# Kernel tuning notes

Hardware: AMD Instinct MI355X
Metric: run time of the kernel (lower is better)

## Reference

```python
import jax, jax.numpy as jnp
import numpy as np

N, E, F_IN, H, OUT, G = 40000, 640000, 128, 128, 10, 256


def setup_inputs() -> dict:
    key = jax.random.key(0)
    ks = jax.random.split(key, 8)
    x = jax.random.normal(ks[0], (N, F_IN), dtype=jnp.float32)
    edge_index = jax.random.randint(ks[1], (2, E), 0, N, dtype=jnp.int32)
    batch = jnp.sort(jax.random.randint(ks[2], (N,), 0, G, dtype=jnp.int32))
    W1 = jax.random.normal(ks[3], (F_IN, H), dtype=jnp.float32) / np.sqrt(F_IN)
    b1 = jnp.zeros((H,), dtype=jnp.float32)
    W2 = jax.random.normal(ks[4], (H, H), dtype=jnp.float32) / np.sqrt(H)
    b2 = jnp.zeros((H,), dtype=jnp.float32)
    Wfc = jax.random.normal(ks[5], (H, OUT), dtype=jnp.float32) / np.sqrt(H)
    bfc = jnp.zeros((OUT,), dtype=jnp.float32)
    return {"x": x, "edge_index": edge_index, "batch": batch,
            "W1": W1, "b1": b1, "W2": W2, "b2": b2, "Wfc": Wfc, "bfc": bfc}


def _gcn_conv(x, W, b, row, col, num_nodes):
    # x' = D^{-1/2} (A+I) D^{-1/2} (x W) + b   (self-loops already in row/col)
    xw = x @ W                                            # [N, H]
    ones = jnp.ones(row.shape[0], dtype=x.dtype)
    deg = jax.ops.segment_sum(ones, col, num_segments=num_nodes)
    dinv = jnp.where(deg > 0, jax.lax.rsqrt(jnp.maximum(deg, 1.0)), 0.0)
    norm = dinv[row] * dinv[col]                          # [E+N]
    msg = xw[row] * norm[:, None]                         # gather + scale
    return jax.ops.segment_sum(msg, col, num_segments=num_nodes) + b


def reference(x, edge_index, batch, W1, b1, W2, b2, Wfc, bfc):
    num_nodes = x.shape[0]
    loop = jnp.arange(num_nodes, dtype=edge_index.dtype)
    row = jnp.concatenate([edge_index[0], loop])
    col = jnp.concatenate([edge_index[1], loop])

    h = jax.nn.relu(_gcn_conv(x, W1, b1, row, col, num_nodes))
    h = jax.nn.relu(_gcn_conv(h, W2, b2, row, col, num_nodes))

    # global_mean_pool over graph ids
    sums = jax.ops.segment_sum(h, batch, num_segments=G)  # [G, H]
    cnt = jax.ops.segment_sum(jnp.ones(num_nodes, h.dtype), batch, num_segments=G)
    pooled = sums / jnp.maximum(cnt, 1.0)[:, None]

    logits = pooled @ Wfc + bfc                           # [G, OUT]
    return jax.nn.log_softmax(logits, axis=-1)
```

## Files before the change

### kernel.cpp

```cpp
#include <hip/hip_runtime.h>
#include <math.h>

#define H_DIM 128
#define OUT_DIM 10

typedef __attribute__((ext_vector_type(8))) __bf16 bf16x8;
typedef __attribute__((ext_vector_type(8))) unsigned short ushort8;
typedef __attribute__((ext_vector_type(4))) float f32x4;

__device__ inline unsigned short f2bf_rne(float f) {
    unsigned int u = __float_as_uint(f);
    unsigned int r = u + 0x7FFFu + ((u >> 16) & 1u);
    return (unsigned short)(r >> 16);
}
__device__ inline float bf_lo(unsigned int u) { return __uint_as_float(u << 16); }
__device__ inline float bf_hi(unsigned int u) { return __uint_as_float(u & 0xFFFF0000u); }

#define ACC4(gv, nv) do { \
    const unsigned int* _u = (const unsigned int*)&(gv); \
    ax[0] += bf_lo(_u[0]) * (nv); ay[0] += bf_hi(_u[0]) * (nv); \
    ax[1] += bf_lo(_u[1]) * (nv); ay[1] += bf_hi(_u[1]) * (nv); \
    ax[2] += bf_lo(_u[2]) * (nv); ay[2] += bf_hi(_u[2]) * (nv); \
    ax[3] += bf_lo(_u[3]) * (nv); ay[3] += bf_hi(_u[3]) * (nv); \
} while (0)

__device__ inline void gather_node(const int4* __restrict__ XW16,
                                   const int2* __restrict__ csr,
                                   int start, int end, int c, float dc2,
                                   int sub, int fl, int lane,
                                   float ax[4], float ay[4]) {
    {
        float s = (sub == 0) ? dc2 : 0.0f;
        int4 gs = XW16[(size_t)c * 16 + fl];
        const unsigned int* u = (const unsigned int*)&gs;
        ax[0] = bf_lo(u[0]) * s; ay[0] = bf_hi(u[0]) * s;
        ax[1] = bf_lo(u[1]) * s; ay[1] = bf_hi(u[1]) * s;
        ax[2] = bf_lo(u[2]) * s; ay[2] = bf_hi(u[2]) * s;
        ax[3] = bf_lo(u[3]) * s; ay[3] = bf_hi(u[3]) * s;
    }
    for (int base = start; base < end; base += 64) {
        int m = end - base; if (m > 64) m = 64;
        int2 ce; ce.x = c; ce.y = 0;
        if (lane < m) ce = csr[base + lane];
        int groups = (m + 3) >> 2;
        int g = 0;
        for (; g + 3 < groups; g += 4) {
            int j = g * 4 + sub;
            int r0 = __shfl(ce.x, j);      float n0 = __int_as_float(__shfl(ce.y, j));
            int r1 = __shfl(ce.x, j + 4);  float n1 = __int_as_float(__shfl(ce.y, j + 4));
            int r2 = __shfl(ce.x, j + 8);  float n2 = __int_as_float(__shfl(ce.y, j + 8));
            int r3 = __shfl(ce.x, j + 12); float n3 = __int_as_float(__shfl(ce.y, j + 12));
            int4 g0 = XW16[(size_t)r0 * 16 + fl];
            int4 g1 = XW16[(size_t)r1 * 16 + fl];
            int4 g2 = XW16[(size_t)r2 * 16 + fl];
            int4 g3 = XW16[(size_t)r3 * 16 + fl];
            ACC4(g0, n0); ACC4(g1, n1); ACC4(g2, n2); ACC4(g3, n3);
        }
        for (; g < groups; ++g) {
            int j = g * 4 + sub;
            int r = __shfl(ce.x, j); float n = __int_as_float(__shfl(ce.y, j));
            int4 gg = XW16[(size_t)r * 16 + fl];
            ACC4(gg, n);
        }
    }
    #pragma unroll
    for (int q = 0; q < 4; ++q) {
        ax[q] += __shfl_xor(ax[q], 16); ax[q] += __shfl_xor(ax[q], 32);
        ay[q] += __shfl_xor(ay[q], 16); ay[q] += __shfl_xor(ay[q], 32);
    }
}

__global__ __launch_bounds__(256) void prep_kernel(const float* __restrict__ W1,
                                                   const float* __restrict__ W2,
                                                   unsigned short* __restrict__ Wt1Hi,
                                                   unsigned short* __restrict__ Wt1Lo,
                                                   unsigned short* __restrict__ Wt2Hi,
                                                   unsigned short* __restrict__ Wt2Lo,
                                                   int hb,
                                                   const int* __restrict__ col,
                                                   int* __restrict__ cnt,
                                                   int* __restrict__ rank, int E) {
    if (blockIdx.x < (unsigned)hb) {
        int e = blockIdx.x * 256 + threadIdx.x;
        if (e < E) rank[e] = atomicAdd(&cnt[col[e]], 1);
    } else {
        int i = (blockIdx.x - hb) * 256 + threadIdx.x;
        const float* src   = (i < 16384) ? W1    : W2;
        unsigned short* dh = (i < 16384) ? Wt1Hi : Wt2Hi;
        unsigned short* dl = (i < 16384) ? Wt1Lo : Wt2Lo;
        int idx = i & 16383;
        int k = idx >> 7, n = idx & 127;
        float v = src[idx];
        unsigned short hbv = f2bf_rne(v);
        float hf = __uint_as_float((unsigned int)hbv << 16);
        unsigned short lb = f2bf_rne(v - hf);
        dh[n * H_DIM + k] = hbv;
        dl[n * H_DIM + k] = lb;
    }
}

__global__ __launch_bounds__(256) void scan_phase1(const int* __restrict__ cnt,
                                                   int* __restrict__ blockSums,
                                                   float* __restrict__ dinv, int N) {
    __shared__ int red[256];
    int base = blockIdx.x * 1024;
    int t = threadIdx.x;
    int s = 0;
    for (int i = 0; i < 4; ++i) {
        int idx = base + t * 4 + i;
        if (idx < N) {
            int cv = cnt[idx];
            s += cv;
            dinv[idx] = rsqrtf((float)cv + 1.0f);
        }
    }
    red[t] = s;
    __syncthreads();
    for (int d = 128; d > 0; d >>= 1) {
        if (t < d) red[t] += red[t + d];
        __syncthreads();
    }
    if (t == 0) blockSums[blockIdx.x] = red[0];
}

__global__ __launch_bounds__(256) void scan_phase23(const int* __restrict__ cnt,
                                                    const int* __restrict__ blockSums,
                                                    int* __restrict__ offs, int N, int B) {
    __shared__ int red[256];
    __shared__ int bsum[256];
    int base = blockIdx.x * 1024;
    int t = threadIdx.x;

    bsum[t] = (t < B && t < (int)blockIdx.x) ? blockSums[t] : 0;

    int v[4];
    int s = 0;
    for (int i = 0; i < 4; ++i) {
        int idx = base + t * 4 + i;
        v[i] = (idx < N) ? cnt[idx] : 0;
        s += v[i];
    }
    red[t] = s;
    __syncthreads();
    for (int d = 128; d > 0; d >>= 1) {
        if (t < d) bsum[t] += bsum[t + d];
        __syncthreads();
    }
    for (int d = 1; d < 256; d <<= 1) {
        int x = (t >= d) ? red[t - d] : 0;
        __syncthreads();
        red[t] += x;
        __syncthreads();
    }
    int run = bsum[0] + ((t == 0) ? 0 : red[t - 1]);
    for (int i = 0; i < 4; ++i) {
        int idx = base + t * 4 + i;
        if (idx < N) { offs[idx] = run; run += v[i]; }
    }
    if ((int)blockIdx.x == B - 1 && t == 255) offs[N] = run;
}

__global__ __launch_bounds__(256) void scatter_gemm1(
        const int* __restrict__ row, const int* __restrict__ col,
        const int* __restrict__ rank, const float* __restrict__ dinv,
        const int* __restrict__ offs, int2* __restrict__ csr, int E, int sb,
        const float* __restrict__ Xf,
        const unsigned short* __restrict__ WtHi, const unsigned short* __restrict__ WtLo,
        unsigned short* __restrict__ Yb, int N) {
    if (blockIdx.x < (unsigned)sb) {
        int e = blockIdx.x * 256 + threadIdx.x;
        if (e >= E) return;
        int r = row[e], c = col[e], rk = rank[e];
        int pos = offs[c] + rk;
        int2 p; p.x = r; p.y = __float_as_int(dinv[r] * dinv[c]);
        csr[pos] = p;
        return;
    }
    int blk  = blockIdx.x - sb;
    int lane = threadIdx.x & 63;
    int wv   = threadIdx.x >> 6;
    int m16  = lane & 15;
    int quad = lane >> 4;
    int nodeBase = blk * 32;

    f32x4 acc[2][2] = {};

    #pragma unroll
    for (int kt = 0; kt < 4; ++kt) {
        int k0 = kt * 32 + quad * 8;

        ushort8 aHi[2], aLo[2];
        #pragma unroll
        for (int mi = 0; mi < 2; ++mi) {
            int node = nodeBase + mi * 16 + m16;
            if (node >= N) node = N - 1;
            const float* p = Xf + (size_t)node * H_DIM + k0;
            f32x4 u = *(const f32x4*)p;
            f32x4 w = *(const f32x4*)(p + 4);
            float vv[8] = {u.x, u.y, u.z, u.w, w.x, w.y, w.z, w.w};
            #pragma unroll
            for (int j = 0; j < 8; ++j) {
                unsigned short hbv = f2bf_rne(vv[j]);
                aHi[mi][j] = hbv;
                aLo[mi][j] = f2bf_rne(vv[j] - __uint_as_float((unsigned int)hbv << 16));
            }
        }

        ushort8 bHi[2], bLo[2];
        #pragma unroll
        for (int ni = 0; ni < 2; ++ni) {
            int n = (wv * 2 + ni) * 16 + m16;
            size_t off = (size_t)n * H_DIM + k0;
            bHi[ni] = *(const ushort8*)(WtHi + off);
            bLo[ni] = *(const ushort8*)(WtLo + off);
        }

        #pragma unroll
        for (int mi = 0; mi < 2; ++mi)
            #pragma unroll
            for (int ni = 0; ni < 2; ++ni) {
                acc[mi][ni] = __builtin_amdgcn_mfma_f32_16x16x32_bf16(
                    __builtin_bit_cast(bf16x8, aHi[mi]),
                    __builtin_bit_cast(bf16x8, bHi[ni]), acc[mi][ni], 0, 0, 0);
                acc[mi][ni] = __builtin_amdgcn_mfma_f32_16x16x32_bf16(
                    __builtin_bit_cast(bf16x8, aLo[mi]),
                    __builtin_bit_cast(bf16x8, bHi[ni]), acc[mi][ni], 0, 0, 0);
                acc[mi][ni] = __builtin_amdgcn_mfma_f32_16x16x32_bf16(
                    __builtin_bit_cast(bf16x8, aHi[mi]),
                    __builtin_bit_cast(bf16x8, bLo[ni]), acc[mi][ni], 0, 0, 0);
            }
    }

    #pragma unroll
    for (int mi = 0; mi < 2; ++mi)
        #pragma unroll
        for (int r = 0; r < 4; ++r) {
            int node = nodeBase + mi * 16 + quad * 4 + r;
            if (node < N) {
                #pragma unroll
                for (int ni = 0; ni < 2; ++ni) {
                    int c = (wv * 2 + ni) * 16 + m16;
                    Yb[(size_t)node * H_DIM + c] = f2bf_rne(acc[mi][ni][r]);
                }
            }
        }
}

__global__ __launch_bounds__(256) void agg1_gemm2(
        const unsigned short* __restrict__ XWb,
        const float* __restrict__ dinv,
        const int2* __restrict__ csr,
        const int* __restrict__ offs,
        const float* __restrict__ bias,
        const unsigned short* __restrict__ WtHi,
        const unsigned short* __restrict__ WtLo,
        unsigned short* __restrict__ Yb,
        int N) {
    __shared__ __align__(16) unsigned short hrow[16][136];
    int lane = threadIdx.x & 63;
    int wv   = threadIdx.x >> 6;
    int sub  = lane >> 4;
    int fl   = lane & 15;
    int nodeBase = blockIdx.x * 16;
    const int4* XW16 = (const int4*)XWb;
    float4 b0 = ((const float4*)bias)[fl * 2];
    float4 b1 = ((const float4*)bias)[fl * 2 + 1];

    for (int i = 0; i < 4; ++i) {
        int c = nodeBase + wv * 4 + i;
        float ax[4] = {}, ay[4] = {};
        if (c < N) {
            int start = offs[c], end = offs[c + 1];
            float dc = dinv[c];
            gather_node(XW16, csr, start, end, c, dc * dc, sub, fl, lane, ax, ay);
            ax[0] = fmaxf(ax[0] + b0.x, 0.f); ay[0] = fmaxf(ay[0] + b0.y, 0.f);
            ax[1] = fmaxf(ax[1] + b0.z, 0.f); ay[1] = fmaxf(ay[1] + b0.w, 0.f);
            ax[2] = fmaxf(ax[2] + b1.x, 0.f); ay[2] = fmaxf(ay[2] + b1.y, 0.f);
            ax[3] = fmaxf(ax[3] + b1.z, 0.f); ay[3] = fmaxf(ay[3] + b1.w, 0.f);
        }
        if (sub == 0) {
            unsigned int o[4];
            #pragma unroll
            for (int q = 0; q < 4; ++q)
                o[q] = (unsigned int)f2bf_rne(ax[q]) | ((unsigned int)f2bf_rne(ay[q]) << 16);
            *(int4*)&hrow[wv * 4 + i][fl * 8] = *(const int4*)o;
        }
    }
    __syncthreads();

    int m16  = lane & 15;
    int quad = lane >> 4;
    f32x4 acc[2] = {};
    #pragma unroll
    for (int kt = 0; kt < 4; ++kt) {
        int k0 = kt * 32 + quad * 8;
        ushort8 a = *(const ushort8*)&hrow[m16][k0];
        #pragma unroll
        for (int ni = 0; ni < 2; ++ni) {
            int n = (wv * 2 + ni) * 16 + m16;
            size_t off = (size_t)n * H_DIM + k0;
            ushort8 bHi = *(const ushort8*)(WtHi + off);
            ushort8 bLo = *(const ushort8*)(WtLo + off);
            acc[ni] = __builtin_amdgcn_mfma_f32_16x16x32_bf16(
                __builtin_bit_cast(bf16x8, a),
                __builtin_bit_cast(bf16x8, bHi), acc[ni], 0, 0, 0);
            acc[ni] = __builtin_amdgcn_mfma_f32_16x16x32_bf16(
                __builtin_bit_cast(bf16x8, a),
                __builtin_bit_cast(bf16x8, bLo), acc[ni], 0, 0, 0);
        }
    }
    #pragma unroll
    for (int r = 0; r < 4; ++r) {
        int node = nodeBase + quad * 4 + r;
        if (node < N) {
            #pragma unroll
            for (int ni = 0; ni < 2; ++ni) {
                int cc = (wv * 2 + ni) * 16 + m16;
                Yb[(size_t)node * H_DIM + cc] = f2bf_rne(acc[ni][r]);
            }
        }
    }
}

__global__ __launch_bounds__(256) void agg_pool(const unsigned short* __restrict__ XWb,
                                                const float* __restrict__ dinv,
                                                const int2* __restrict__ csr,
                                                const int* __restrict__ offs,
                                                const float* __restrict__ bias,
                                                const int* __restrict__ batch,
                                                float* __restrict__ pooledSum, int N) {
    int wave = (blockIdx.x * 256 + threadIdx.x) >> 6;
    int lane = threadIdx.x & 63;
    int wv   = threadIdx.x >> 6;
    int sub  = lane >> 4;
    int fl   = lane & 15;
    bool active = wave < N;

    float ax[4] = {}, ay[4] = {};
    int c = wave;
    if (active) {
        int start = offs[c], end = offs[c + 1];
        float dc = dinv[c];
        gather_node((const int4*)XWb, csr, start, end, c, dc * dc, sub, fl, lane, ax, ay);
        float4 b0 = ((const float4*)bias)[fl * 2];
        float4 b1 = ((const float4*)bias)[fl * 2 + 1];
        ax[0] = fmaxf(ax[0] + b0.x, 0.f); ay[0] = fmaxf(ay[0] + b0.y, 0.f);
        ax[1] = fmaxf(ax[1] + b0.z, 0.f); ay[1] = fmaxf(ay[1] + b0.w, 0.f);
        ax[2] = fmaxf(ax[2] + b1.x, 0.f); ay[2] = fmaxf(ay[2] + b1.y, 0.f);
        ax[3] = fmaxf(ax[3] + b1.z, 0.f); ay[3] = fmaxf(ay[3] + b1.w, 0.f);
    }

    __shared__ float lacc[4][H_DIM];
    __shared__ int lg[4];
    if (lane == 0) lg[wv] = active ? batch[c] : -1;
    if (sub == 0) {
        float4 f0; f0.x = ax[0]; f0.y = ay[0]; f0.z = ax[1]; f0.w = ay[1];
        float4 f1; f1.x = ax[2]; f1.y = ay[2]; f1.z = ax[3]; f1.w = ay[3];
        ((float4*)&lacc[wv][fl * 8])[0] = f0;
        ((float4*)&lacc[wv][fl * 8])[1] = f1;
    }
    __syncthreads();
    int t = threadIdx.x;
    if (t < H_DIM) {
        float s = 0.f; int cur = -1;
        #pragma unroll
        for (int w = 0; w < 4; ++w) {
            int g = lg[w];
            if (g < 0) continue;
            if (g != cur) {
                if (cur >= 0) atomicAdd(&pooledSum[cur * H_DIM + t], s);
                s = 0.f; cur = g;
            }
            s += lacc[w][t];
        }
        if (cur >= 0) atomicAdd(&pooledSum[cur * H_DIM + t], s);
    }
}

__global__ __launch_bounds__(64) void head_kernel(const float* __restrict__ pooledSum,
                                                  const int* __restrict__ batch,
                                                  const float* __restrict__ Wfc,
                                                  const float* __restrict__ bfc,
                                                  float* __restrict__ out, int N) {
    __shared__ float sl[OUT_DIM + 2];
    __shared__ int bounds[2];
    int g = blockIdx.x;
    int j = threadIdx.x;
    if (j < 2) {
        int v = g + j;
        int lo = 0, hi = N;
        while (lo < hi) {
            int mid = (lo + hi) >> 1;
            if (batch[mid] < v) lo = mid + 1; else hi = mid;
        }
        bounds[j] = lo;
    }
    __syncthreads();
    int cnt = bounds[1] - bounds[0];
    float inv = 1.0f / (float)(cnt > 0 ? cnt : 1);
    if (j < OUT_DIM) {
        float acc = 0.f;
        const float* p = pooledSum + g * H_DIM;
        for (int k = 0; k < H_DIM; ++k) acc += p[k] * Wfc[k * OUT_DIM + j];
        sl[j] = acc * inv + bfc[j];
    }
    __syncthreads();
    if (j == 0) {
        float m = sl[0];
        for (int i = 1; i < OUT_DIM; ++i) m = fmaxf(m, sl[i]);
        float s = 0.f;
        for (int i = 0; i < OUT_DIM; ++i) s += expf(sl[i] - m);
        sl[OUT_DIM] = m + logf(s);
    }
    __syncthreads();
    if (j < OUT_DIM) out[g * OUT_DIM + j] = sl[j] - sl[OUT_DIM];
}

extern "C" void kernel_launch(void* const* d_in, const int* in_sizes, int n_in,
                              void* d_out, int out_size, void* d_ws, size_t ws_size,
                              hipStream_t stream) {
    const float* x     = (const float*)d_in[0];
    const int*   ei    = (const int*)  d_in[1];
    const int*   batch = (const int*)  d_in[2];
    const float* W1    = (const float*)d_in[3];
    const float* b1    = (const float*)d_in[4];
    const float* W2    = (const float*)d_in[5];
    const float* b2    = (const float*)d_in[6];
    const float* Wfc   = (const float*)d_in[7];
    const float* bfc   = (const float*)d_in[8];
    float* out = (float*)d_out;

    int N = in_sizes[2];
    int E = in_sizes[1] / 2;
    int G = out_size / OUT_DIM;
    const int* row = ei;
    const int* col = ei + E;

    char* wsb = (char*)d_ws;
    size_t nAlign = (size_t)((N + 256) / 256) * 256;
    size_t eAlign = (size_t)((E + 255) / 256) * 256;
    int*   cnt       = (int*)wsb;
    float* pooledSum = (float*)(cnt + nAlign);
    int*   offs      = (int*)(pooledSum + (size_t)G * H_DIM);
    int*   rank      = offs + nAlign;
    float* dinv      = (float*)(rank + eAlign);
    int2*  csr       = (int2*)(dinv + nAlign);
    unsigned short* Xb = (unsigned short*)(csr + E);
    unsigned short* Hb = Xb + (size_t)N * H_DIM;
    int* blockSums = (int*)(Hb + (size_t)N * H_DIM);
    unsigned short* Wt1Hi = (unsigned short*)(blockSums + 256);
    unsigned short* Wt1Lo = Wt1Hi + H_DIM * H_DIM;
    unsigned short* Wt2Hi = Wt1Lo + H_DIM * H_DIM;
    unsigned short* Wt2Lo = Wt2Hi + H_DIM * H_DIM;

    int scanBlocks = (N + 1023) / 1024;
    int histBlocks = (E + 255) / 256;
    int gemmBlocks = (N + 31) / 32;

    hipMemsetAsync(cnt, 0, (nAlign + (size_t)G * H_DIM) * sizeof(int), stream);

    prep_kernel<<<histBlocks + 128, 256, 0, stream>>>(
        W1, W2, Wt1Hi, Wt1Lo, Wt2Hi, Wt2Lo, histBlocks, col, cnt, rank, E);

    scan_phase1<<<scanBlocks, 256, 0, stream>>>(cnt, blockSums, dinv, N);
    scan_phase23<<<scanBlocks, 256, 0, stream>>>(cnt, blockSums, offs, N, scanBlocks);

    scatter_gemm1<<<histBlocks + gemmBlocks, 256, 0, stream>>>(
        row, col, rank, dinv, offs, csr, E, histBlocks,
        x, Wt1Hi, Wt1Lo, Xb, N);

    int ag1Blocks = (N + 15) / 16;
    agg1_gemm2<<<ag1Blocks, 256, 0, stream>>>(Xb, dinv, csr, offs, b1,
                                              Wt2Hi, Wt2Lo, Hb, N);

    int aggBlocks = (N + 3) / 4;
    agg_pool<<<aggBlocks, 256, 0, stream>>>(Hb, dinv, csr, offs, b2,
                                            batch, pooledSum, N);

    head_kernel<<<G, 64, 0, stream>>>(pooledSum, batch, Wfc, bfc, out, N);
}
```

Baseline: 222.3 us.

## Pack CSR entries into 32-bit index+fp16 norm and restructure agg1_gemm2 per-wave nodes

CSR entries are packed into one 32-bit word: the source index sits in the upper 16 bits and the edge norm is stored as fp16 in the lower 16 bits. This halves the CSR traffic in the scatter and in both aggregation kernels. agg1_gemm2 now uses 512-thread blocks with one node per wave, and the MFMA tile is zero-padded to 16 rows. The packing only holds for fewer than 65536 nodes and lowers norm precision to fp16, and the padded MFMA wastes half of its rows.

```diff
diff --git a/kernel.cpp b/kernel.cpp
--- a/kernel.cpp
+++ b/kernel.cpp
@@ -1,4 +1,5 @@
 #include <hip/hip_runtime.h>
+#include <hip/hip_fp16.h>
 #include <math.h>
 
 #define H_DIM 128
@@ -15,6 +16,9 @@
 }
 __device__ inline float bf_lo(unsigned int u) { return __uint_as_float(u << 16); }
 __device__ inline float bf_hi(unsigned int u) { return __uint_as_float(u & 0xFFFF0000u); }
+__device__ inline float h2f(unsigned int e) {
+    return __half2float(__ushort_as_half((unsigned short)(e & 0xFFFFu)));
+}
 
 #define ACC4(gv, nv) do { \
     const unsigned int* _u = (const unsigned int*)&(gv); \
@@ -25,7 +29,7 @@
 } while (0)
 
 __device__ inline void gather_node(const int4* __restrict__ XW16,
-                                   const int2* __restrict__ csr,
+                                   const unsigned int* __restrict__ csr,
                                    int start, int end, int c, float dc2,
                                    int sub, int fl, int lane,
                                    float ax[4], float ay[4]) {
@@ -40,26 +44,28 @@
     }
     for (int base = start; base < end; base += 64) {
         int m = end - base; if (m > 64) m = 64;
-        int2 ce; ce.x = c; ce.y = 0;
+        unsigned int ce = ((unsigned int)c) << 16;
         if (lane < m) ce = csr[base + lane];
         int groups = (m + 3) >> 2;
         int g = 0;
         for (; g + 3 < groups; g += 4) {
             int j = g * 4 + sub;
-            int r0 = __shfl(ce.x, j);      float n0 = __int_as_float(__shfl(ce.y, j));
-            int r1 = __shfl(ce.x, j + 4);  float n1 = __int_as_float(__shfl(ce.y, j + 4));
-            int r2 = __shfl(ce.x, j + 8);  float n2 = __int_as_float(__shfl(ce.y, j + 8));
-            int r3 = __shfl(ce.x, j + 12); float n3 = __int_as_float(__shfl(ce.y, j + 12));
-            int4 g0 = XW16[(size_t)r0 * 16 + fl];
-            int4 g1 = XW16[(size_t)r1 * 16 + fl];
-            int4 g2 = XW16[(size_t)r2 * 16 + fl];
-            int4 g3 = XW16[(size_t)r3 * 16 + fl];
+            unsigned int e0 = __shfl((int)ce, j);
+            unsigned int e1 = __shfl((int)ce, j + 4);
+            unsigned int e2 = __shfl((int)ce, j + 8);
+            unsigned int e3 = __shfl((int)ce, j + 12);
+            int4 g0 = XW16[(size_t)(e0 >> 16) * 16 + fl];
+            int4 g1 = XW16[(size_t)(e1 >> 16) * 16 + fl];
+            int4 g2 = XW16[(size_t)(e2 >> 16) * 16 + fl];
+            int4 g3 = XW16[(size_t)(e3 >> 16) * 16 + fl];
+            float n0 = h2f(e0), n1 = h2f(e1), n2 = h2f(e2), n3 = h2f(e3);
             ACC4(g0, n0); ACC4(g1, n1); ACC4(g2, n2); ACC4(g3, n3);
         }
         for (; g < groups; ++g) {
             int j = g * 4 + sub;
-            int r = __shfl(ce.x, j); float n = __int_as_float(__shfl(ce.y, j));
-            int4 gg = XW16[(size_t)r * 16 + fl];
+            unsigned int e = __shfl((int)ce, j);
+            int4 gg = XW16[(size_t)(e >> 16) * 16 + fl];
+            float n = h2f(e);
             ACC4(gg, n);
         }
     }
@@ -163,7 +169,7 @@
 __global__ __launch_bounds__(256) void scatter_gemm1(
         const int* __restrict__ row, const int* __restrict__ col,
         const int* __restrict__ rank, const float* __restrict__ dinv,
-        const int* __restrict__ offs, int2* __restrict__ csr, int E, int sb,
+        const int* __restrict__ offs, unsigned int* __restrict__ csr, int E, int sb,
         const float* __restrict__ Xf,
         const unsigned short* __restrict__ WtHi, const unsigned short* __restrict__ WtLo,
         unsigned short* __restrict__ Yb, int N) {
@@ -172,8 +178,9 @@
         if (e >= E) return;
         int r = row[e], c = col[e], rk = rank[e];
         int pos = offs[c] + rk;
-        int2 p; p.x = r; p.y = __float_as_int(dinv[r] * dinv[c]);
-        csr[pos] = p;
+        float norm = dinv[r] * dinv[c];
+        unsigned short nb = __half_as_ushort(__float2half(norm));
+        csr[pos] = (((unsigned int)r) << 16) | nb;
         return;
     }
     int blk  = blockIdx.x - sb;
@@ -246,10 +253,10 @@
         }
 }
 
-__global__ __launch_bounds__(256) void agg1_gemm2(
+__global__ __launch_bounds__(512, 8) void agg1_gemm2(
         const unsigned short* __restrict__ XWb,
         const float* __restrict__ dinv,
-        const int2* __restrict__ csr,
+        const unsigned int* __restrict__ csr,
         const int* __restrict__ offs,
         const float* __restrict__ bias,
         const unsigned short* __restrict__ WtHi,
@@ -261,70 +268,63 @@
     int wv   = threadIdx.x >> 6;
     int sub  = lane >> 4;
     int fl   = lane & 15;
-    int nodeBase = blockIdx.x * 16;
+    int nodeBase = blockIdx.x * 8;
+    int c = nodeBase + wv;
     const int4* XW16 = (const int4*)XWb;
-    float4 b0 = ((const float4*)bias)[fl * 2];
-    float4 b1 = ((const float4*)bias)[fl * 2 + 1];
-
-    for (int i = 0; i < 4; ++i) {
-        int c = nodeBase + wv * 4 + i;
-        float ax[4] = {}, ay[4] = {};
-        if (c < N) {
-            int start = offs[c], end = offs[c + 1];
-            float dc = dinv[c];
-            gather_node(XW16, csr, start, end, c, dc * dc, sub, fl, lane, ax, ay);
-            ax[0] = fmaxf(ax[0] + b0.x, 0.f); ay[0] = fmaxf(ay[0] + b0.y, 0.f);
-            ax[1] = fmaxf(ax[1] + b0.z, 0.f); ay[1] = fmaxf(ay[1] + b0.w, 0.f);
-            ax[2] = fmaxf(ax[2] + b1.x, 0.f); ay[2] = fmaxf(ay[2] + b1.y, 0.f);
-            ax[3] = fmaxf(ax[3] + b1.z, 0.f); ay[3] = fmaxf(ay[3] + b1.w, 0.f);
-        }
-        if (sub == 0) {
-            unsigned int o[4];
-            #pragma unroll
-            for (int q = 0; q < 4; ++q)
-                o[q] = (unsigned int)f2bf_rne(ax[q]) | ((unsigned int)f2bf_rne(ay[q]) << 16);
-            *(int4*)&hrow[wv * 4 + i][fl * 8] = *(const int4*)o;
-        }
+
+    float ax[4] = {}, ay[4] = {};
+    if (c < N) {
+        int start = offs[c], end = offs[c + 1];
+        float dc = dinv[c];
+        gather_node(XW16, csr, start, end, c, dc * dc, sub, fl, lane, ax, ay);
+        float4 b0 = ((const float4*)bias)[fl * 2];
+        float4 b1 = ((const float4*)bias)[fl * 2 + 1];
+        ax[0] = fmaxf(ax[0] + b0.x, 0.f); ay[0] = fmaxf(ay[0] + b0.y, 0.f);
+        ax[1] = fmaxf(ax[1] + b0.z, 0.f); ay[1] = fmaxf(ay[1] + b0.w, 0.f);
+        ax[2] = fmaxf(ax[2] + b1.x, 0.f); ay[2] = fmaxf(ay[2] + b1.y, 0.f);
+        ax[3] = fmaxf(ax[3] + b1.z, 0.f); ay[3] = fmaxf(ay[3] + b1.w, 0.f);
+    }
+    if (sub == 0) {
+        unsigned int o[4];
+        #pragma unroll
+        for (int q = 0; q < 4; ++q)
+            o[q] = (unsigned int)f2bf_rne(ax[q]) | ((unsigned int)f2bf_rne(ay[q]) << 16);
+        *(int4*)&hrow[wv][fl * 8] = *(const int4*)o;
+        int4 z; z.x = 0; z.y = 0; z.z = 0; z.w = 0;
+        *(int4*)&hrow[wv + 8][fl * 8] = z;
     }
     __syncthreads();
 
     int m16  = lane & 15;
     int quad = lane >> 4;
-    f32x4 acc[2] = {};
+    f32x4 acc = {};
     #pragma unroll
     for (int kt = 0; kt < 4; ++kt) {
         int k0 = kt * 32 + quad * 8;
         ushort8 a = *(const ushort8*)&hrow[m16][k0];
-        #pragma unroll
-        for (int ni = 0; ni < 2; ++ni) {
-            int n = (wv * 2 + ni) * 16 + m16;
-            size_t off = (size_t)n * H_DIM + k0;
-            ushort8 bHi = *(const ushort8*)(WtHi + off);
-            ushort8 bLo = *(const ushort8*)(WtLo + off);
-            acc[ni] = __builtin_amdgcn_mfma_f32_16x16x32_bf16(
-                __builtin_bit_cast(bf16x8, a),
-                __builtin_bit_cast(bf16x8, bHi), acc[ni], 0, 0, 0);
-            acc[ni] = __builtin_amdgcn_mfma_f32_16x16x32_bf16(
-                __builtin_bit_cast(bf16x8, a),
-                __builtin_bit_cast(bf16x8, bLo), acc[ni], 0, 0, 0);
-        }
+        int n = wv * 16 + m16;
+        size_t off = (size_t)n * H_DIM + k0;
+        ushort8 bHi = *(const ushort8*)(WtHi + off);
+        ushort8 bLo = *(const ushort8*)(WtLo + off);
+        acc = __builtin_amdgcn_mfma_f32_16x16x32_bf16(
+            __builtin_bit_cast(bf16x8, a), __builtin_bit_cast(bf16x8, bHi), acc, 0, 0, 0);
+        acc = __builtin_amdgcn_mfma_f32_16x16x32_bf16(
+            __builtin_bit_cast(bf16x8, a), __builtin_bit_cast(bf16x8, bLo), acc, 0, 0, 0);
     }
     #pragma unroll
     for (int r = 0; r < 4; ++r) {
-        int node = nodeBase + quad * 4 + r;
-        if (node < N) {
-            #pragma unroll
-            for (int ni = 0; ni < 2; ++ni) {
-                int cc = (wv * 2 + ni) * 16 + m16;
-                Yb[(size_t)node * H_DIM + cc] = f2bf_rne(acc[ni][r]);
-            }
+        int rw = quad * 4 + r;
+        if (rw < 8) {
+            int node = nodeBase + rw;
+            if (node < N)
+                Yb[(size_t)node * H_DIM + wv * 16 + m16] = f2bf_rne(acc[r]);
         }
     }
 }
 
 __global__ __launch_bounds__(256) void agg_pool(const unsigned short* __restrict__ XWb,
                                                 const float* __restrict__ dinv,
-                                                const int2* __restrict__ csr,
+                                                const unsigned int* __restrict__ csr,
                                                 const int* __restrict__ offs,
                                                 const float* __restrict__ bias,
                                                 const int* __restrict__ batch,
@@ -444,8 +444,8 @@
     int*   offs      = (int*)(pooledSum + (size_t)G * H_DIM);
     int*   rank      = offs + nAlign;
     float* dinv      = (float*)(rank + eAlign);
-    int2*  csr       = (int2*)(dinv + nAlign);
-    unsigned short* Xb = (unsigned short*)(csr + E);
+    unsigned int* csr = (unsigned int*)(dinv + nAlign);
+    unsigned short* Xb = (unsigned short*)(csr + eAlign);
     unsigned short* Hb = Xb + (size_t)N * H_DIM;
     int* blockSums = (int*)(Hb + (size_t)N * H_DIM);
     unsigned short* Wt1Hi = (unsigned short*)(blockSums + 256);
@@ -469,8 +469,8 @@
         row, col, rank, dinv, offs, csr, E, histBlocks,
         x, Wt1Hi, Wt1Lo, Xb, N);
 
-    int ag1Blocks = (N + 15) / 16;
-    agg1_gemm2<<<ag1Blocks, 256, 0, stream>>>(Xb, dinv, csr, offs, b1,
+    int ag1Blocks = (N + 7) / 8;
+    agg1_gemm2<<<ag1Blocks, 512, 0, stream>>>(Xb, dinv, csr, offs, b1,
                                               Wt2Hi, Wt2Lo, Hb, N);
 
     int aggBlocks = (N + 3) / 4;
```

New measurement: 241.2 us. +8.5%, slower.

## Pack CSR entries into 32-bit row|fp16 norm and prefetch edge segments

Applied to the files above, without the earlier changes.

Each CSR edge entry shrinks from an int2 (row index plus fp32 norm) to a single 32-bit word holding a 16-bit row index and an fp16 norm, halving CSR traffic and shuffle count in the gather loops. agg1_gemm2 now loads the offsets, the first 64-edge CSR segment and the self-row features for all four nodes up front, so these loads are in flight before any gathering starts. Packing the row into 16 bits only works when N is below 65536 (N is 40000 here), and the fp16 norm loses precision compared with fp32.

```diff
diff --git a/kernel.cpp b/kernel.cpp
--- a/kernel.cpp
+++ b/kernel.cpp
@@ -1,4 +1,5 @@
 #include <hip/hip_runtime.h>
+#include <hip/hip_fp16.h>
 #include <math.h>
 
 #define H_DIM 128
@@ -15,6 +16,9 @@
 }
 __device__ inline float bf_lo(unsigned int u) { return __uint_as_float(u << 16); }
 __device__ inline float bf_hi(unsigned int u) { return __uint_as_float(u & 0xFFFF0000u); }
+__device__ inline float h2f(unsigned int e) {
+    return __half2float(__ushort_as_half((unsigned short)(e & 0xFFFFu)));
+}
 
 #define ACC4(gv, nv) do { \
     const unsigned int* _u = (const unsigned int*)&(gv); \
@@ -24,50 +28,70 @@
     ax[3] += bf_lo(_u[3]) * (nv); ay[3] += bf_hi(_u[3]) * (nv); \
 } while (0)
 
-__device__ inline void gather_node(const int4* __restrict__ XW16,
-                                   const int2* __restrict__ csr,
-                                   int start, int end, int c, float dc2,
-                                   int sub, int fl, int lane,
-                                   float ax[4], float ay[4]) {
+#define SEG_BODY(ce, m) do { \
+    int groups = ((m) + 3) >> 2; \
+    int g = 0; \
+    for (; g + 3 < groups; g += 4) { \
+        int j = g * 4 + sub; \
+        unsigned int e0 = __shfl((int)(ce), j); \
+        unsigned int e1 = __shfl((int)(ce), j + 4); \
+        unsigned int e2 = __shfl((int)(ce), j + 8); \
+        unsigned int e3 = __shfl((int)(ce), j + 12); \
+        int4 g0 = XW16[(size_t)(e0 >> 16) * 16 + fl]; \
+        int4 g1 = XW16[(size_t)(e1 >> 16) * 16 + fl]; \
+        int4 g2 = XW16[(size_t)(e2 >> 16) * 16 + fl]; \
+        int4 g3 = XW16[(size_t)(e3 >> 16) * 16 + fl]; \
+        float n0 = h2f(e0), n1 = h2f(e1), n2 = h2f(e2), n3 = h2f(e3); \
+        ACC4(g0, n0); ACC4(g1, n1); ACC4(g2, n2); ACC4(g3, n3); \
+    } \
+    for (; g < groups; ++g) { \
+        int j = g * 4 + sub; \
+        unsigned int e = __shfl((int)(ce), j); \
+        int4 gg = XW16[(size_t)(e >> 16) * 16 + fl]; \
+        float n = h2f(e); \
+        ACC4(gg, n); \
+    } \
+} while (0)
+
+__device__ inline void gather_node_pre(const int4* __restrict__ XW16,
+                                       const unsigned int* __restrict__ csr,
+                                       int start, int end, int c, float dc2,
+                                       unsigned int ce0, int4 gs,
+                                       int sub, int fl, int lane,
+                                       float ax[4], float ay[4]) {
     {
         float s = (sub == 0) ? dc2 : 0.0f;
-        int4 gs = XW16[(size_t)c * 16 + fl];
         const unsigned int* u = (const unsigned int*)&gs;
         ax[0] = bf_lo(u[0]) * s; ay[0] = bf_hi(u[0]) * s;
         ax[1] = bf_lo(u[1]) * s; ay[1] = bf_hi(u[1]) * s;
         ax[2] = bf_lo(u[2]) * s; ay[2] = bf_hi(u[2]) * s;
         ax[3] = bf_lo(u[3]) * s; ay[3] = bf_hi(u[3]) * s;
     }
-    for (int base = start; base < end; base += 64) {
+    int m0 = end - start; if (m0 > 64) m0 = 64;
+    SEG_BODY(ce0, m0);
+    for (int base = start + 64; base < end; base += 64) {
         int m = end - base; if (m > 64) m = 64;
-        int2 ce; ce.x = c; ce.y = 0;
+        unsigned int ce = ((unsigned int)c) << 16;
         if (lane < m) ce = csr[base + lane];
-        int groups = (m + 3) >> 2;
-        int g = 0;
-        for (; g + 3 < groups; g += 4) {
-            int j = g * 4 + sub;
-            int r0 = __shfl(ce.x, j);      float n0 = __int_as_float(__shfl(ce.y, j));
-            int r1 = __shfl(ce.x, j + 4);  float n1 = __int_as_float(__shfl(ce.y, j + 4));
-            int r2 = __shfl(ce.x, j + 8);  float n2 = __int_as_float(__shfl(ce.y, j + 8));
-            int r3 = __shfl(ce.x, j + 12); float n3 = __int_as_float(__shfl(ce.y, j + 12));
-            int4 g0 = XW16[(size_t)r0 * 16 + fl];
-            int4 g1 = XW16[(size_t)r1 * 16 + fl];
-            int4 g2 = XW16[(size_t)r2 * 16 + fl];
-            int4 g3 = XW16[(size_t)r3 * 16 + fl];
-            ACC4(g0, n0); ACC4(g1, n1); ACC4(g2, n2); ACC4(g3, n3);
-        }
-        for (; g < groups; ++g) {
-            int j = g * 4 + sub;
-            int r = __shfl(ce.x, j); float n = __int_as_float(__shfl(ce.y, j));
-            int4 gg = XW16[(size_t)r * 16 + fl];
-            ACC4(gg, n);
-        }
+        SEG_BODY(ce, m);
     }
     #pragma unroll
     for (int q = 0; q < 4; ++q) {
         ax[q] += __shfl_xor(ax[q], 16); ax[q] += __shfl_xor(ax[q], 32);
         ay[q] += __shfl_xor(ay[q], 16); ay[q] += __shfl_xor(ay[q], 32);
     }
+}
+
+__device__ inline void gather_node(const int4* __restrict__ XW16,
+                                   const unsigned int* __restrict__ csr,
+                                   int start, int end, int c, float dc2,
+                                   int sub, int fl, int lane,
+                                   float ax[4], float ay[4]) {
+    int m0 = end - start; if (m0 > 64) m0 = 64;
+    unsigned int ce0 = ((unsigned int)c) << 16;
+    if (lane < m0) ce0 = csr[start + lane];
+    int4 gs = XW16[(size_t)c * 16 + fl];
+    gather_node_pre(XW16, csr, start, end, c, dc2, ce0, gs, sub, fl, lane, ax, ay);
 }
 
 __global__ __launch_bounds__(256) void prep_kernel(const float* __restrict__ W1,
@@ -163,7 +187,7 @@
 __global__ __launch_bounds__(256) void scatter_gemm1(
         const int* __restrict__ row, const int* __restrict__ col,
         const int* __restrict__ rank, const float* __restrict__ dinv,
-        const int* __restrict__ offs, int2* __restrict__ csr, int E, int sb,
+        const int* __restrict__ offs, unsigned int* __restrict__ csr, int E, int sb,
         const float* __restrict__ Xf,
         const unsigned short* __restrict__ WtHi, const unsigned short* __restrict__ WtLo,
         unsigned short* __restrict__ Yb, int N) {
@@ -172,8 +196,9 @@
         if (e >= E) return;
         int r = row[e], c = col[e], rk = rank[e];
         int pos = offs[c] + rk;
-        int2 p; p.x = r; p.y = __float_as_int(dinv[r] * dinv[c]);
-        csr[pos] = p;
+        float norm = dinv[r] * dinv[c];
+        unsigned short nb = __half_as_ushort(__float2half(norm));
+        csr[pos] = (((unsigned int)r) << 16) | nb;
         return;
     }
     int blk  = blockIdx.x - sb;
@@ -249,7 +274,7 @@
 __global__ __launch_bounds__(256) void agg1_gemm2(
         const unsigned short* __restrict__ XWb,
         const float* __restrict__ dinv,
-        const int2* __restrict__ csr,
+        const unsigned int* __restrict__ csr,
         const int* __restrict__ offs,
         const float* __restrict__ bias,
         const unsigned short* __restrict__ WtHi,
@@ -266,18 +291,37 @@
     float4 b0 = ((const float4*)bias)[fl * 2];
     float4 b1 = ((const float4*)bias)[fl * 2 + 1];
 
+    int cN[4], st[4], en[4];
+    float dc2[4];
+    #pragma unroll
     for (int i = 0; i < 4; ++i) {
         int c = nodeBase + wv * 4 + i;
-        float ax[4] = {}, ay[4] = {};
-        if (c < N) {
-            int start = offs[c], end = offs[c + 1];
-            float dc = dinv[c];
-            gather_node(XW16, csr, start, end, c, dc * dc, sub, fl, lane, ax, ay);
-            ax[0] = fmaxf(ax[0] + b0.x, 0.f); ay[0] = fmaxf(ay[0] + b0.y, 0.f);
-            ax[1] = fmaxf(ax[1] + b0.z, 0.f); ay[1] = fmaxf(ay[1] + b0.w, 0.f);
-            ax[2] = fmaxf(ax[2] + b1.x, 0.f); ay[2] = fmaxf(ay[2] + b1.y, 0.f);
-            ax[3] = fmaxf(ax[3] + b1.z, 0.f); ay[3] = fmaxf(ay[3] + b1.w, 0.f);
-        }
+        bool ok = c < N;
+        int cc = ok ? c : N - 1;
+        cN[i] = cc;
+        st[i] = ok ? offs[cc] : 0;
+        en[i] = ok ? offs[cc + 1] : 0;
+        float d = dinv[cc];
+        dc2[i] = ok ? d * d : 0.f;
+    }
+    unsigned int ce0[4]; int4 gs[4];
+    #pragma unroll
+    for (int i = 0; i < 4; ++i) {
+        int m = en[i] - st[i]; if (m > 64) m = 64;
+        unsigned int pad = ((unsigned int)cN[i]) << 16;
+        ce0[i] = (lane < m) ? csr[st[i] + lane] : pad;
+        gs[i] = XW16[(size_t)cN[i] * 16 + fl];
+    }
+
+    #pragma unroll
+    for (int i = 0; i < 4; ++i) {
+        float ax[4], ay[4];
+        gather_node_pre(XW16, csr, st[i], en[i], cN[i], dc2[i],
+                        ce0[i], gs[i], sub, fl, lane, ax, ay);
+        ax[0] = fmaxf(ax[0] + b0.x, 0.f); ay[0] = fmaxf(ay[0] + b0.y, 0.f);
+        ax[1] = fmaxf(ax[1] + b0.z, 0.f); ay[1] = fmaxf(ay[1] + b0.w, 0.f);
+        ax[2] = fmaxf(ax[2] + b1.x, 0.f); ay[2] = fmaxf(ay[2] + b1.y, 0.f);
+        ax[3] = fmaxf(ax[3] + b1.z, 0.f); ay[3] = fmaxf(ay[3] + b1.w, 0.f);
         if (sub == 0) {
             unsigned int o[4];
             #pragma unroll
@@ -324,7 +368,7 @@
 
 __global__ __launch_bounds__(256) void agg_pool(const unsigned short* __restrict__ XWb,
                                                 const float* __restrict__ dinv,
-                                                const int2* __restrict__ csr,
+                                                const unsigned int* __restrict__ csr,
                                                 const int* __restrict__ offs,
                                                 const float* __restrict__ bias,
                                                 const int* __restrict__ batch,
@@ -444,8 +488,8 @@
     int*   offs      = (int*)(pooledSum + (size_t)G * H_DIM);
     int*   rank      = offs + nAlign;
     float* dinv      = (float*)(rank + eAlign);
-    int2*  csr       = (int2*)(dinv + nAlign);
-    unsigned short* Xb = (unsigned short*)(csr + E);
+    unsigned int* csr = (unsigned int*)(dinv + nAlign);
+    unsigned short* Xb = (unsigned short*)(csr + eAlign);
     unsigned short* Hb = Xb + (size_t)N * H_DIM;
     int* blockSums = (int*)(Hb + (size_t)N * H_DIM);
     unsigned short* Wt1Hi = (unsigned short*)(blockSums + 256);
```

After: 224.1 us. About the same (+0.8%).
